# Optimization experiments

Measured on AMD Instinct MI355X. Metric: run time of the kernel, lower is better.

## Reference

```python
import jax, jax.numpy as jnp
import numpy as np
import math

B, S, U, H = 2, 2048, 1024, 16
DK = U // H  # 64


def setup_inputs() -> dict:
    key = jax.random.key(0)
    ks = jax.random.split(key, 12)
    scale = 1.0 / math.sqrt(U)
    inp = {
        "query": jax.random.normal(ks[0], (B, S, U), dtype=jnp.float32),
        "key": jax.random.normal(ks[1], (B, S, U), dtype=jnp.float32),
        "value": jax.random.normal(ks[2], (B, S, U), dtype=jnp.float32),
        # causal mask, broadcast over batch: 1 = attend, 0 = masked
        "mask": jnp.broadcast_to(jnp.tril(jnp.ones((S, S), dtype=bool)), (B, S, S)),
        # nn.Linear params (torch convention: y = x @ W.T + b)
        "Wq": jax.random.uniform(ks[3], (U, U), jnp.float32, -scale, scale),
        "bq": jax.random.uniform(ks[4], (U,), jnp.float32, -scale, scale),
        "Wk": jax.random.uniform(ks[5], (U, U), jnp.float32, -scale, scale),
        "bk": jax.random.uniform(ks[6], (U,), jnp.float32, -scale, scale),
        "Wv": jax.random.uniform(ks[7], (U, U), jnp.float32, -scale, scale),
        "bv": jax.random.uniform(ks[8], (U,), jnp.float32, -scale, scale),
        "Wo": jax.random.uniform(ks[9], (U, U), jnp.float32, -scale, scale),
        "bo": jax.random.uniform(ks[10], (U,), jnp.float32, -scale, scale),
    }
    return inp


def reference(query, key, value, mask, Wq, bq, Wk, bk, Wv, bv, Wo, bo):
    b = query.shape[0]
    # QKV projections -> [b, H, S, DK]
    q = (query @ Wq.T + bq).reshape(b, -1, H, DK).transpose(0, 2, 1, 3)
    k = (key @ Wk.T + bk).reshape(b, -1, H, DK).transpose(0, 2, 1, 3)
    v = (value @ Wv.T + bv).reshape(b, -1, H, DK).transpose(0, 2, 1, 3)
    # scaled dot-product scores [b, H, Sq, Sk]
    scores = jnp.einsum("bhqd,bhkd->bhqk", q, k) / math.sqrt(DK)
    scores = jnp.where(mask[:, None, :, :], scores, jnp.float32(-1e9))
    A = jax.nn.softmax(scores, axis=-1)
    # dropout is eval/identity (p effectively inactive in reference)
    Hout = jnp.einsum("bhqk,bhkd->bhqd", A, v)
    H_concat = Hout.transpose(0, 2, 1, 3).reshape(b, -1, U)
    return H_concat @ Wo.T + bo
```

## Files before the change

kernel.cpp:

```cpp
#include <hip/hip_runtime.h>
#include <math.h>

#define B_NUM 2
#define S_LEN 2048
#define U_DIM 1024
#define H_NUM 16
#define DK 64
#define M_TOT (B_NUM * S_LEN)

typedef __attribute__((ext_vector_type(8))) short bf8;
typedef __attribute__((ext_vector_type(4))) float f4;

__device__ __forceinline__ unsigned short f2bf(float f) {
    union { float f; unsigned int u; } x; x.f = f;
    unsigned int r = x.u + 0x7fffu + ((x.u >> 16) & 1u);
    return (unsigned short)(r >> 16);
}

__device__ __forceinline__ unsigned int pkbf(float a, float b) {
    unsigned int r;
    asm("v_cvt_pk_bf16_f32 %0, %1, %2" : "=v"(r) : "v"(a), "v"(b));
    return r;
}

__device__ __forceinline__ void gl2lds16(const void* g, void* l) {
    __builtin_amdgcn_global_load_lds(
        (const __attribute__((address_space(1))) unsigned int*)g,
        (__attribute__((address_space(3))) unsigned int*)l, 16, 0, 0);
}

struct CvtArgs {
    const float* src[7];
    unsigned short* dst[7];
    int n[7];
};

__global__ __launch_bounds__(256) void convert_bf16(CvtArgs a)
{
    const int seg = blockIdx.y;
    const int i = (blockIdx.x * 256 + threadIdx.x) * 8;
    if (i >= a.n[seg]) return;
    const float* s = a.src[seg] + i;
    float4 v0 = *(const float4*)s;
    float4 v1 = *(const float4*)(s + 4);
    uint4 o = {pkbf(v0.x, v0.y), pkbf(v0.z, v0.w),
               pkbf(v1.x, v1.y), pkbf(v1.z, v1.w)};
    *(uint4*)(a.dst[seg] + i) = o;
}

struct GemmLds {
    unsigned short As[2][128][32];
    unsigned short Bs[2][128][32];
};

template <int OMODE>
__device__ __forceinline__ void gemm_core(
    GemmLds& S,
    const unsigned short* __restrict__ A, const unsigned short* __restrict__ W,
    const float* __restrict__ bias, void* __restrict__ Cv, float scale,
    int bx, int by)
{
    const int tid = threadIdx.x;
    const int w = tid >> 6, lane = tid & 63;
    const int quad = lane >> 4, cid = lane & 15;
    const int wy = w >> 1, wx = w & 1;
    const int m0 = by * 128, n0 = bx * 128;

    const int l2 = lane >> 2, s4 = lane & 3;
    const int ra = 32 * w + l2;
    const int rr = (ra >> 2) & 3;
    const int cseg = (((s4 + 4) - rr) & 3) * 8;
    const unsigned short* gAs = A + (size_t)(m0 + ra) * U_DIM + cseg;
    const unsigned short* gBs = W + (size_t)(n0 + ra) * U_DIM + cseg;

#define STAGE(buf_, k_) do {                                               \
        gl2lds16(gAs + (k_),              &S.As[buf_][32 * w][0]);         \
        gl2lds16(gAs + (k_) + 16 * U_DIM, &S.As[buf_][32 * w + 16][0]);    \
        gl2lds16(gBs + (k_),              &S.Bs[buf_][32 * w][0]);         \
        gl2lds16(gBs + (k_) + 16 * U_DIM, &S.Bs[buf_][32 * w + 16][0]);    \
    } while (0)

    f4 acc[4][4] = {};

    STAGE(0, 0);

#pragma unroll 2
    for (int k0 = 0; k0 < U_DIM; k0 += 32) {
        const int cur = (k0 >> 5) & 1;
        __syncthreads();
        if (k0 + 32 < U_DIM) STAGE(cur ^ 1, k0 + 32);

        bf8 af[4], bfr[4];
#pragma unroll
        for (int mt = 0; mt < 4; ++mt) {
            int row = wy * 64 + mt * 16 + cid;
            int seg = (quad + (row >> 2)) & 3;
            af[mt] = *(const bf8*)&S.As[cur][row][seg * 8];
        }
#pragma unroll
        for (int nt = 0; nt < 4; ++nt) {
            int row = wx * 64 + nt * 16 + cid;
            int seg = (quad + (row >> 2)) & 3;
            bfr[nt] = *(const bf8*)&S.Bs[cur][row][seg * 8];
        }
#pragma unroll
        for (int mt = 0; mt < 4; ++mt)
#pragma unroll
            for (int nt = 0; nt < 4; ++nt)
                acc[mt][nt] = __builtin_amdgcn_mfma_f32_16x16x32_bf16(
                    af[mt], bfr[nt], acc[mt][nt], 0, 0, 0);
    }
#undef STAGE

#pragma unroll
    for (int nt = 0; nt < 4; ++nt) {
        int col = n0 + wx * 64 + nt * 16 + cid;
        float bv = bias[col];
#pragma unroll
        for (int mt = 0; mt < 4; ++mt) {
            int rowb = m0 + wy * 64 + mt * 16 + quad * 4;
#pragma unroll
            for (int i = 0; i < 4; ++i) {
                float v = (acc[mt][nt][i] + bv) * scale;
                if constexpr (OMODE == 0) {
                    ((unsigned short*)Cv)[(size_t)(rowb + i) * U_DIM + col] = f2bf(v);
                } else if constexpr (OMODE == 1) {
                    ((float*)Cv)[(size_t)(rowb + i) * U_DIM + col] = v;
                } else {
                    int bb = rowb >> 11;
                    int ss = (rowb & (S_LEN - 1)) + i;
                    size_t idx = ((size_t)(bb * H_NUM + (col >> 6)) * DK + (col & 63))
                                 * S_LEN + ss;
                    ((unsigned short*)Cv)[idx] = f2bf(v);
                }
            }
        }
    }
}

struct QkvArgs {
    const unsigned short* A[3];
    const unsigned short* W[3];
    const float* bias[3];
    unsigned short* C[3];
    float scale[3];
};

__global__ __launch_bounds__(256, 3) void gemm_qkv(QkvArgs a) {
    __shared__ GemmLds S;
    const int L = (int)blockIdx.x + 8 * ((int)blockIdx.y + 32 * (int)blockIdx.z);
    const int xcd = L & 7, j = L >> 3;
    const int z = j >> 5, r = j & 31;
    const int by = xcd * 4 + (r & 3);
    const int bx = r >> 2;
    if (z == 2)
        gemm_core<2>(S, a.A[2], a.W[2], a.bias[2], a.C[2], a.scale[2], bx, by);
    else
        gemm_core<0>(S, a.A[z], a.W[z], a.bias[z], a.C[z], a.scale[z], bx, by);
}

__global__ __launch_bounds__(256, 3) void gemm_obf(
    const unsigned short* __restrict__ A, const unsigned short* __restrict__ W,
    const float* __restrict__ bias, float* __restrict__ C) {
    __shared__ GemmLds S;
    const int L = (int)blockIdx.x + 8 * (int)blockIdx.y;
    const int xcd = L & 7, j = L >> 3;
    const int by = xcd * 4 + (j & 3);
    const int bx = j >> 2;
    gemm_core<1>(S, A, W, bias, C, 1.0f, bx, by);
}

__global__ __launch_bounds__(256, 4) void attn_mfma(
    const unsigned short* __restrict__ Q, const unsigned short* __restrict__ K,
    const unsigned short* __restrict__ VT, unsigned short* __restrict__ O)
{
    __shared__ __align__(16) unsigned short Ks[128][64];
    __shared__ __align__(16) unsigned short Vs[64][128];

    const int L = (int)blockIdx.x + 32 * ((int)blockIdx.y + 16 * (int)blockIdx.z);
    const int xcd = L & 7;
    const int j   = L >> 3;
    const int gl  = j & 3;
    const int i   = j >> 2;
    const int hb  = (xcd << 2) | gl;
    const int h = hb & 15, b = hb >> 4;
    const int px = i & 7, pk = i >> 3;
    const int qt = (pk == 0) ? 31 - px : (pk == 1) ? 16 + px
                 : (pk == 2) ? 15 - px : px;

    const int q0 = qt * 64;
    const int tid = threadIdx.x, w = tid >> 6, lane = tid & 63;
    const int quad = lane >> 4, cid = lane & 15;

#define KFRAG(r, s) (*(const bf8*)&Ks[r][(((s) ^ ((r) & 7)) * 8)])
#define VFRAG(r, s) (*(const bf8*)&Vs[r][(((((s) & 8) | (((s) ^ (r)) & 7))) * 8)])

    unsigned short (*QsA)[64] = (unsigned short (*)[64])&Ks[0][0];
    const int srow8 = lane >> 3;
    const int sw = ((lane & 7) ^ srow8) * 8;
    {
        const unsigned short* qg =
            Q + ((size_t)b * S_LEN + q0 + w * 16 + srow8) * U_DIM + h * DK + sw;
        gl2lds16(qg, &QsA[w * 16][0]);
        gl2lds16(qg + 8 * U_DIM, &QsA[w * 16 + 8][0]);
    }
    __syncthreads();
    const bf8 qfa = *(const bf8*)&QsA[w * 16 + cid][(((quad) ^ (cid & 7)) * 8)];
    const bf8 qfb = *(const bf8*)&QsA[w * 16 + cid][((((quad + 4)) ^ (cid & 7)) * 8)];

    const unsigned short* kgl =
        K + ((size_t)b * S_LEN + w * 32 + srow8) * U_DIM + h * DK + (lane & 7) * 8;
    const int vr0 = lane >> 4;
    const int s16 = lane & 15;
    const unsigned short* vgl =
        VT + ((size_t)(b * H_NUM + h) * DK + w * 16 + vr0) * S_LEN + s16 * 8;
    const int spE = (((s16 & 8) | ((s16 ^ vr0) & 7))) * 8;
    const int spO = (((s16 & 8) | ((s16 ^ (vr0 + 4)) & 7))) * 8;
    const int ksw = ((lane & 7) ^ srow8) * 8;

    uint4 kr0, kr1, kr2, kr3, vq0, vq1, vq2, vq3;
#define PREFETCH(kt_) do {                                                    \
        const unsigned short* kp_ = kgl + (size_t)(kt_) * 128 * U_DIM;        \
        kr0 = *(const uint4*)(kp_);                                           \
        kr1 = *(const uint4*)(kp_ + (size_t)8 * U_DIM);                       \
        kr2 = *(const uint4*)(kp_ + (size_t)16 * U_DIM);                      \
        kr3 = *(const uint4*)(kp_ + (size_t)24 * U_DIM);                      \
        const unsigned short* vp_ = vgl + (kt_) * 128;                        \
        vq0 = *(const uint4*)(vp_);                                           \
        vq1 = *(const uint4*)(vp_ + (size_t)4 * S_LEN);                       \
        vq2 = *(const uint4*)(vp_ + (size_t)8 * S_LEN);                       \
        vq3 = *(const uint4*)(vp_ + (size_t)12 * S_LEN);                      \
    } while (0)

    f4 o[4] = {};
    float l_p = 0.0f;
    const int qrow = q0 + w * 16 + cid;

    const int nkt = (qt >> 1) + 1;
    PREFETCH(0);

    for (int kt = 0; kt < nkt; ++kt) {
        __syncthreads();
        *(uint4*)&Ks[w * 32 + 0  + srow8][ksw] = kr0;
        *(uint4*)&Ks[w * 32 + 8  + srow8][ksw] = kr1;
        *(uint4*)&Ks[w * 32 + 16 + srow8][ksw] = kr2;
        *(uint4*)&Ks[w * 32 + 24 + srow8][ksw] = kr3;
        *(uint4*)&Vs[w * 16 + 0  + vr0][spE] = vq0;
        *(uint4*)&Vs[w * 16 + 4  + vr0][spO] = vq1;
        *(uint4*)&Vs[w * 16 + 8  + vr0][spE] = vq2;
        *(uint4*)&Vs[w * 16 + 12 + vr0][spO] = vq3;
        __syncthreads();
        if (kt + 1 < nkt) PREFETCH(kt + 1);

        f4 sc[8];
#pragma unroll
        for (int t = 0; t < 8; ++t) {
            int r = t * 16 + cid;
            f4 a = {};
            a = __builtin_amdgcn_mfma_f32_16x16x32_bf16(KFRAG(r, quad), qfa, a, 0, 0, 0);
            a = __builtin_amdgcn_mfma_f32_16x16x32_bf16(KFRAG(r, quad + 4), qfb, a, 0, 0, 0);
            sc[t] = a;
        }

        if (kt == nkt - 1) {
#pragma unroll
            for (int t = 0; t < 8; ++t) {
#pragma unroll
                for (int i2 = 0; i2 < 4; ++i2) {
                    int key = kt * 128 + t * 16 + quad * 4 + i2;
                    if (key > qrow) sc[t][i2] = -1e30f;
                }
            }
        }

#pragma unroll
        for (int t = 0; t < 8; ++t) {
#pragma unroll
            for (int i2 = 0; i2 < 4; ++i2) {
                float p = exp2f(sc[t][i2]);
                sc[t][i2] = p;
                l_p += p;
            }
        }

        unsigned int r_[8], r2_[8];
#pragma unroll
        for (int t = 0; t < 8; ++t) {
            r_[t]  = pkbf(sc[t][0], sc[t][1]);
            r2_[t] = pkbf(sc[t][2], sc[t][3]);
        }

        const bool qodd = (quad & 1) != 0;
#pragma unroll
        for (int f = 0; f < 4; ++f) {
            unsigned int xa = r_[2 * f], ya = r_[2 * f + 1];
            asm("v_permlane32_swap_b32 %0, %1" : "+v"(xa), "+v"(ya));
            unsigned int xas = __builtin_amdgcn_ds_swizzle((int)xa, 0x401f);
            unsigned int yas = __builtin_amdgcn_ds_swizzle((int)ya, 0x401f);
            unsigned int xb = r2_[2 * f], yb = r2_[2 * f + 1];
            asm("v_permlane32_swap_b32 %0, %1" : "+v"(xb), "+v"(yb));
            unsigned int xbs = __builtin_amdgcn_ds_swizzle((int)xb, 0x401f);
            unsigned int ybs = __builtin_amdgcn_ds_swizzle((int)yb, 0x401f);
            unsigned int u0 = qodd ? yas : xa;
            unsigned int u1 = qodd ? ybs : xb;
            unsigned int u2 = qodd ? ya : xas;
            unsigned int u3 = qodd ? yb : xbs;
            union { uint4 u; bf8 v; } pf;
            pf.u = (uint4){u0, u1, u2, u3};
#pragma unroll
            for (int t = 0; t < 4; ++t) {
                int r = t * 16 + cid;
                o[t] = __builtin_amdgcn_mfma_f32_16x16x32_bf16(
                    pf.v, VFRAG(r, 4 * f + quad), o[t], 0, 0, 0);
            }
        }
    }
#undef PREFETCH
#undef KFRAG
#undef VFRAG

    float l = l_p;
    l += __shfl_xor(l, 16);
    l += __shfl_xor(l, 32);
    const float inv = 1.0f / l;
#pragma unroll
    for (int i2 = 0; i2 < 4; ++i2) {
        float invi = __shfl(inv, (lane & 48) | (quad * 4 + i2));
        int rowg = q0 + w * 16 + quad * 4 + i2;
        size_t rbase = ((size_t)b * S_LEN + rowg) * U_DIM + h * DK;
#pragma unroll
        for (int t = 0; t < 4; ++t)
            O[rbase + t * 16 + cid] = f2bf(o[t][i2] * invi);
    }
}

extern "C" void kernel_launch(void* const* d_in, const int* in_sizes, int n_in,
                              void* d_out, int out_size, void* d_ws, size_t ws_size,
                              hipStream_t stream)
{
    const float* query = (const float*)d_in[0];
    const float* key   = (const float*)d_in[1];
    const float* value = (const float*)d_in[2];
    const float* Wq = (const float*)d_in[4];
    const float* bq = (const float*)d_in[5];
    const float* Wk = (const float*)d_in[6];
    const float* bk = (const float*)d_in[7];
    const float* Wv = (const float*)d_in[8];
    const float* bv = (const float*)d_in[9];
    const float* Wo = (const float*)d_in[10];
    const float* bo = (const float*)d_in[11];
    float* out = (float*)d_out;

    const size_t ACT = (size_t)M_TOT * U_DIM;
    const size_t WT  = (size_t)U_DIM * U_DIM;

    unsigned short* xq  = (unsigned short*)d_ws;
    unsigned short* xk  = xq + ACT;
    unsigned short* xv  = xk + ACT;
    unsigned short* wqb = xv + ACT;
    unsigned short* wkb = wqb + WT;
    unsigned short* wvb = wkb + WT;
    unsigned short* wob = wvb + WT;
    unsigned short* qg  = wob + WT;
    unsigned short* kg  = qg + ACT;
    unsigned short* vt  = kg + ACT;
    unsigned short* ao  = vt + ACT;

    CvtArgs ca;
    ca.src[0] = query; ca.dst[0] = xq;  ca.n[0] = (int)ACT;
    ca.src[1] = key;   ca.dst[1] = xk;  ca.n[1] = (int)ACT;
    ca.src[2] = value; ca.dst[2] = xv;  ca.n[2] = (int)ACT;
    ca.src[3] = Wq;    ca.dst[3] = wqb; ca.n[3] = (int)WT;
    ca.src[4] = Wk;    ca.dst[4] = wkb; ca.n[4] = (int)WT;
    ca.src[5] = Wv;    ca.dst[5] = wvb; ca.n[5] = (int)WT;
    ca.src[6] = Wo;    ca.dst[6] = wob; ca.n[6] = (int)WT;
    convert_bf16<<<dim3(ACT / (256 * 8), 7), 256, 0, stream>>>(ca);

    QkvArgs ga;
    ga.A[0] = xq; ga.W[0] = wqb; ga.bias[0] = bq; ga.C[0] = qg;
    ga.scale[0] = 0.125f * 1.44269504088896340736f;
    ga.A[1] = xk; ga.W[1] = wkb; ga.bias[1] = bk; ga.C[1] = kg; ga.scale[1] = 1.0f;
    ga.A[2] = xv; ga.W[2] = wvb; ga.bias[2] = bv; ga.C[2] = vt; ga.scale[2] = 1.0f;
    gemm_qkv<<<dim3(U_DIM / 128, M_TOT / 128, 3), 256, 0, stream>>>(ga);

    attn_mfma<<<dim3(S_LEN / 64, H_NUM, B_NUM), 256, 0, stream>>>(qg, kg, vt, ao);

    gemm_obf<<<dim3(U_DIM / 128, M_TOT / 128), 256, 0, stream>>>(ao, wob, bo, out);
}
```

Measured before the change: 224.9 us.

## Fuse convert, QKV GEMM, attention and output GEMM into one cooperative kernel

Merges the four kernel launches into one persistent cooperative kernel of 1024 blocks. Grid-wide syncs separate the bf16 conversion, the QKV projection, attention and the output projection. This removes per-launch overhead and the gaps between kernels. In exchange, blocks sit idle during the GEMM phases (only 768 or 256 of 1024 have work), and the fused kernel is bound by the larger LDS/register footprint at 4 blocks per CU. A fallback path launches separate kernels if the cooperative launch fails, but it converts with only 64 blocks.

```diff
diff --git a/kernel.cpp b/kernel.cpp
--- a/kernel.cpp
+++ b/kernel.cpp
@@ -1,5 +1,8 @@
 #include <hip/hip_runtime.h>
+#include <hip/hip_cooperative_groups.h>
 #include <math.h>
+
+namespace cg = cooperative_groups;
 
 #define B_NUM 2
 #define S_LEN 2048
@@ -35,17 +38,20 @@
     int n[7];
 };
 
-__global__ __launch_bounds__(256) void convert_bf16(CvtArgs a)
+__device__ __forceinline__ void convert_core(const CvtArgs& a, int gtid, int gsz)
 {
-    const int seg = blockIdx.y;
-    const int i = (blockIdx.x * 256 + threadIdx.x) * 8;
-    if (i >= a.n[seg]) return;
-    const float* s = a.src[seg] + i;
-    float4 v0 = *(const float4*)s;
-    float4 v1 = *(const float4*)(s + 4);
-    uint4 o = {pkbf(v0.x, v0.y), pkbf(v0.z, v0.w),
-               pkbf(v1.x, v1.y), pkbf(v1.z, v1.w)};
-    *(uint4*)(a.dst[seg] + i) = o;
+#pragma unroll
+    for (int seg = 0; seg < 7; ++seg) {
+        const int nv = a.n[seg] >> 3;
+        for (int i = gtid; i < nv; i += gsz) {
+            const float* s = a.src[seg] + (size_t)i * 8;
+            float4 v0 = *(const float4*)s;
+            float4 v1 = *(const float4*)(s + 4);
+            uint4 o = {pkbf(v0.x, v0.y), pkbf(v0.z, v0.w),
+                       pkbf(v1.x, v1.y), pkbf(v1.z, v1.w)};
+            *(uint4*)(a.dst[seg] + (size_t)i * 8) = o;
+        }
+    }
 }
 
 struct GemmLds {
@@ -146,38 +152,16 @@
     float scale[3];
 };
 
-__global__ __launch_bounds__(256, 3) void gemm_qkv(QkvArgs a) {
-    __shared__ GemmLds S;
-    const int L = (int)blockIdx.x + 8 * ((int)blockIdx.y + 32 * (int)blockIdx.z);
-    const int xcd = L & 7, j = L >> 3;
-    const int z = j >> 5, r = j & 31;
-    const int by = xcd * 4 + (r & 3);
-    const int bx = r >> 2;
-    if (z == 2)
-        gemm_core<2>(S, a.A[2], a.W[2], a.bias[2], a.C[2], a.scale[2], bx, by);
-    else
-        gemm_core<0>(S, a.A[z], a.W[z], a.bias[z], a.C[z], a.scale[z], bx, by);
-}
-
-__global__ __launch_bounds__(256, 3) void gemm_obf(
-    const unsigned short* __restrict__ A, const unsigned short* __restrict__ W,
-    const float* __restrict__ bias, float* __restrict__ C) {
-    __shared__ GemmLds S;
-    const int L = (int)blockIdx.x + 8 * (int)blockIdx.y;
-    const int xcd = L & 7, j = L >> 3;
-    const int by = xcd * 4 + (j & 3);
-    const int bx = j >> 2;
-    gemm_core<1>(S, A, W, bias, C, 1.0f, bx, by);
-}
-
-__global__ __launch_bounds__(256, 4) void attn_mfma(
+struct AttnLds {
+    unsigned short Ks[128][64];
+    unsigned short Vs[64][128];
+};
+
+__device__ __forceinline__ void attn_core(
+    AttnLds& AL, int L,
     const unsigned short* __restrict__ Q, const unsigned short* __restrict__ K,
     const unsigned short* __restrict__ VT, unsigned short* __restrict__ O)
 {
-    __shared__ __align__(16) unsigned short Ks[128][64];
-    __shared__ __align__(16) unsigned short Vs[64][128];
-
-    const int L = (int)blockIdx.x + 32 * ((int)blockIdx.y + 16 * (int)blockIdx.z);
     const int xcd = L & 7;
     const int j   = L >> 3;
     const int gl  = j & 3;
@@ -192,10 +176,10 @@
     const int tid = threadIdx.x, w = tid >> 6, lane = tid & 63;
     const int quad = lane >> 4, cid = lane & 15;
 
-#define KFRAG(r, s) (*(const bf8*)&Ks[r][(((s) ^ ((r) & 7)) * 8)])
-#define VFRAG(r, s) (*(const bf8*)&Vs[r][(((((s) & 8) | (((s) ^ (r)) & 7))) * 8)])
-
-    unsigned short (*QsA)[64] = (unsigned short (*)[64])&Ks[0][0];
+#define KFRAG(r, s) (*(const bf8*)&AL.Ks[r][(((s) ^ ((r) & 7)) * 8)])
+#define VFRAG(r, s) (*(const bf8*)&AL.Vs[r][(((((s) & 8) | (((s) ^ (r)) & 7))) * 8)])
+
+    unsigned short (*QsA)[64] = (unsigned short (*)[64])&AL.Ks[0][0];
     const int srow8 = lane >> 3;
     const int sw = ((lane & 7) ^ srow8) * 8;
     {
@@ -241,14 +225,14 @@
 
     for (int kt = 0; kt < nkt; ++kt) {
         __syncthreads();
-        *(uint4*)&Ks[w * 32 + 0  + srow8][ksw] = kr0;
-        *(uint4*)&Ks[w * 32 + 8  + srow8][ksw] = kr1;
-        *(uint4*)&Ks[w * 32 + 16 + srow8][ksw] = kr2;
-        *(uint4*)&Ks[w * 32 + 24 + srow8][ksw] = kr3;
-        *(uint4*)&Vs[w * 16 + 0  + vr0][spE] = vq0;
-        *(uint4*)&Vs[w * 16 + 4  + vr0][spO] = vq1;
-        *(uint4*)&Vs[w * 16 + 8  + vr0][spE] = vq2;
-        *(uint4*)&Vs[w * 16 + 12 + vr0][spO] = vq3;
+        *(uint4*)&AL.Ks[w * 32 + 0  + srow8][ksw] = kr0;
+        *(uint4*)&AL.Ks[w * 32 + 8  + srow8][ksw] = kr1;
+        *(uint4*)&AL.Ks[w * 32 + 16 + srow8][ksw] = kr2;
+        *(uint4*)&AL.Ks[w * 32 + 24 + srow8][ksw] = kr3;
+        *(uint4*)&AL.Vs[w * 16 + 0  + vr0][spE] = vq0;
+        *(uint4*)&AL.Vs[w * 16 + 4  + vr0][spO] = vq1;
+        *(uint4*)&AL.Vs[w * 16 + 8  + vr0][spE] = vq2;
+        *(uint4*)&AL.Vs[w * 16 + 12 + vr0][spO] = vq3;
         __syncthreads();
         if (kt + 1 < nkt) PREFETCH(kt + 1);
 
@@ -332,6 +316,93 @@
         for (int t = 0; t < 4; ++t)
             O[rbase + t * 16 + cid] = f2bf(o[t][i2] * invi);
     }
+}
+
+struct FusedArgs {
+    CvtArgs cvt;
+    QkvArgs qkv;
+    const unsigned short *Qg, *Kg, *VTg;
+    unsigned short* Og;
+    const unsigned short* Ao;
+    const unsigned short* Wob;
+    const float* bo;
+    float* outp;
+};
+
+__global__ __launch_bounds__(256, 4) void fused_all(FusedArgs a)
+{
+    __shared__ __align__(16) unsigned char LDSRAW[32768];
+    const int L = (int)blockIdx.x;
+
+    convert_core(a.cvt, L * 256 + (int)threadIdx.x, (int)gridDim.x * 256);
+    cg::this_grid().sync();
+
+    {
+        const int xcd = L & 7, j = L >> 3;
+        if (j < 96) {
+            GemmLds& S = *(GemmLds*)LDSRAW;
+            const int z = j >> 5, r = j & 31;
+            const int by = xcd * 4 + (r & 3);
+            const int bx = r >> 2;
+            if (z == 2)
+                gemm_core<2>(S, a.qkv.A[2], a.qkv.W[2], a.qkv.bias[2],
+                             a.qkv.C[2], a.qkv.scale[2], bx, by);
+            else
+                gemm_core<0>(S, a.qkv.A[z], a.qkv.W[z], a.qkv.bias[z],
+                             a.qkv.C[z], a.qkv.scale[z], bx, by);
+        }
+    }
+    cg::this_grid().sync();
+
+    attn_core(*(AttnLds*)LDSRAW, L, a.Qg, a.Kg, a.VTg, a.Og);
+    cg::this_grid().sync();
+
+    {
+        const int xcd = L & 7, j = L >> 3;
+        if (j < 32) {
+            GemmLds& S = *(GemmLds*)LDSRAW;
+            const int by = xcd * 4 + (j & 3);
+            const int bx = j >> 2;
+            gemm_core<1>(S, a.Ao, a.Wob, a.bo, a.outp, 1.0f, bx, by);
+        }
+    }
+}
+
+__global__ __launch_bounds__(256) void convert_bf16(CvtArgs a) {
+    convert_core(a, (int)(blockIdx.x * 256 + threadIdx.x),
+                 (int)gridDim.x * 256);
+}
+
+__global__ __launch_bounds__(256, 3) void gemm_qkv(QkvArgs a) {
+    __shared__ GemmLds S;
+    const int L = (int)blockIdx.x + 8 * ((int)blockIdx.y + 32 * (int)blockIdx.z);
+    const int xcd = L & 7, j = L >> 3;
+    const int z = j >> 5, r = j & 31;
+    const int by = xcd * 4 + (r & 3);
+    const int bx = r >> 2;
+    if (z == 2)
+        gemm_core<2>(S, a.A[2], a.W[2], a.bias[2], a.C[2], a.scale[2], bx, by);
+    else
+        gemm_core<0>(S, a.A[z], a.W[z], a.bias[z], a.C[z], a.scale[z], bx, by);
+}
+
+__global__ __launch_bounds__(256, 3) void gemm_obf(
+    const unsigned short* __restrict__ A, const unsigned short* __restrict__ W,
+    const float* __restrict__ bias, float* __restrict__ C) {
+    __shared__ GemmLds S;
+    const int L = (int)blockIdx.x + 8 * (int)blockIdx.y;
+    const int xcd = L & 7, j = L >> 3;
+    const int by = xcd * 4 + (j & 3);
+    const int bx = j >> 2;
+    gemm_core<1>(S, A, W, bias, C, 1.0f, bx, by);
+}
+
+__global__ __launch_bounds__(256, 4) void attn_mfma(
+    const unsigned short* __restrict__ Q, const unsigned short* __restrict__ K,
+    const unsigned short* __restrict__ VT, unsigned short* __restrict__ O) {
+    __shared__ AttnLds AL;
+    const int L = (int)blockIdx.x + 32 * ((int)blockIdx.y + 16 * (int)blockIdx.z);
+    attn_core(AL, L, Q, K, VT, O);
 }
 
 extern "C" void kernel_launch(void* const* d_in, const int* in_sizes, int n_in,
@@ -366,24 +437,33 @@
     unsigned short* vt  = kg + ACT;
     unsigned short* ao  = vt + ACT;
 
-    CvtArgs ca;
-    ca.src[0] = query; ca.dst[0] = xq;  ca.n[0] = (int)ACT;
-    ca.src[1] = key;   ca.dst[1] = xk;  ca.n[1] = (int)ACT;
-    ca.src[2] = value; ca.dst[2] = xv;  ca.n[2] = (int)ACT;
-    ca.src[3] = Wq;    ca.dst[3] = wqb; ca.n[3] = (int)WT;
-    ca.src[4] = Wk;    ca.dst[4] = wkb; ca.n[4] = (int)WT;
-    ca.src[5] = Wv;    ca.dst[5] = wvb; ca.n[5] = (int)WT;
-    ca.src[6] = Wo;    ca.dst[6] = wob; ca.n[6] = (int)WT;
-    convert_bf16<<<dim3(ACT / (256 * 8), 7), 256, 0, stream>>>(ca);
-
-    QkvArgs ga;
-    ga.A[0] = xq; ga.W[0] = wqb; ga.bias[0] = bq; ga.C[0] = qg;
-    ga.scale[0] = 0.125f * 1.44269504088896340736f;
-    ga.A[1] = xk; ga.W[1] = wkb; ga.bias[1] = bk; ga.C[1] = kg; ga.scale[1] = 1.0f;
-    ga.A[2] = xv; ga.W[2] = wvb; ga.bias[2] = bv; ga.C[2] = vt; ga.scale[2] = 1.0f;
-    gemm_qkv<<<dim3(U_DIM / 128, M_TOT / 128, 3), 256, 0, stream>>>(ga);
-
-    attn_mfma<<<dim3(S_LEN / 64, H_NUM, B_NUM), 256, 0, stream>>>(qg, kg, vt, ao);
-
-    gemm_obf<<<dim3(U_DIM / 128, M_TOT / 128), 256, 0, stream>>>(ao, wob, bo, out);
-}
+    FusedArgs fa;
+    fa.cvt.src[0] = query; fa.cvt.dst[0] = xq;  fa.cvt.n[0] = (int)ACT;
+    fa.cvt.src[1] = key;   fa.cvt.dst[1] = xk;  fa.cvt.n[1] = (int)ACT;
+    fa.cvt.src[2] = value; fa.cvt.dst[2] = xv;  fa.cvt.n[2] = (int)ACT;
+    fa.cvt.src[3] = Wq;    fa.cvt.dst[3] = wqb; fa.cvt.n[3] = (int)WT;
+    fa.cvt.src[4] = Wk;    fa.cvt.dst[4] = wkb; fa.cvt.n[4] = (int)WT;
+    fa.cvt.src[5] = Wv;    fa.cvt.dst[5] = wvb; fa.cvt.n[5] = (int)WT;
+    fa.cvt.src[6] = Wo;    fa.cvt.dst[6] = wob; fa.cvt.n[6] = (int)WT;
+
+    fa.qkv.A[0] = xq; fa.qkv.W[0] = wqb; fa.qkv.bias[0] = bq; fa.qkv.C[0] = qg;
+    fa.qkv.scale[0] = 0.125f * 1.44269504088896340736f;
+    fa.qkv.A[1] = xk; fa.qkv.W[1] = wkb; fa.qkv.bias[1] = bk; fa.qkv.C[1] = kg;
+    fa.qkv.scale[1] = 1.0f;
+    fa.qkv.A[2] = xv; fa.qkv.W[2] = wvb; fa.qkv.bias[2] = bv; fa.qkv.C[2] = vt;
+    fa.qkv.scale[2] = 1.0f;
+
+    fa.Qg = qg; fa.Kg = kg; fa.VTg = vt; fa.Og = ao;
+    fa.Ao = ao; fa.Wob = wob; fa.bo = bo; fa.outp = out;
+
+    void* kargs[] = { (void*)&fa };
+    hipError_t e = hipLaunchCooperativeKernel(
+        (const void*)fused_all, dim3(1024), dim3(256), kargs, 0, stream);
+
+    if (e != hipSuccess) {
+        convert_bf16<<<dim3(64, 1), 256, 0, stream>>>(fa.cvt);
+        gemm_qkv<<<dim3(8, 32, 3), 256, 0, stream>>>(fa.qkv);
+        attn_mfma<<<dim3(32, 16, 2), 256, 0, stream>>>(qg, kg, vt, ao);
+        gemm_obf<<<dim3(8, 32), 256, 0, stream>>>(ao, wob, bo, out);
+    }
+}
```

Measured after the change: 620.6 us. +175.9%, slower.
